# Optimization experiments

Hardware: AMD Instinct MI355X
Metric: run time of the kernel (lower is better)

The kernel has to match this reference:

```python
import jax, jax.numpy as jnp
import numpy as np

N_NODES = 100000
N_EDGES = 1600000
F_IN = 64
HIDDEN = 64
N_CLASSES = 2


def setup_inputs() -> dict:
    key = jax.random.key(0)
    k1, k2, k3, k4, k5, k6 = jax.random.split(key, 6)
    x = jax.random.normal(k1, (N_NODES, F_IN), dtype=jnp.float32)
    edge_index = jax.random.randint(k2, (2, N_EDGES), 0, N_NODES, dtype=jnp.int64)
    # Glorot-ish init for GCNConv linear weights, zero bias (PyG default)
    W1 = jax.random.normal(k3, (F_IN, HIDDEN), dtype=jnp.float32) * (1.0 / np.sqrt(F_IN))
    b1 = jnp.zeros((HIDDEN,), dtype=jnp.float32)
    W2 = jax.random.normal(k4, (HIDDEN, N_CLASSES), dtype=jnp.float32) * (1.0 / np.sqrt(HIDDEN))
    b2 = jnp.zeros((N_CLASSES,), dtype=jnp.float32)
    return {"x": x, "edge_index": edge_index, "W1": W1, "b1": b1, "W2": W2, "b2": b2}


def _gcn_norm(edge_index, num_nodes):
    # Add self-loops, then symmetric normalization D^-1/2 (A+I) D^-1/2
    loops = jnp.arange(num_nodes, dtype=edge_index.dtype)
    row = jnp.concatenate([edge_index[0], loops])  # [E+N] targets
    col = jnp.concatenate([edge_index[1], loops])  # [E+N] sources
    deg = jax.ops.segment_sum(jnp.ones(row.shape[0], jnp.float32), row, num_segments=num_nodes)
    dinv = jnp.where(deg > 0, jax.lax.rsqrt(deg), 0.0)
    norm = dinv[row] * dinv[col]  # [E+N]
    return row, col, norm


def _gcn_conv(x, W, b, row, col, norm, num_nodes):
    h = x @ W                                   # [N, out]
    msg = h[col] * norm[:, None]                # gather + scale, [E+N, out]
    agg = jax.ops.segment_sum(msg, row, num_segments=num_nodes)  # scatter-add
    return agg + b


def reference(x, edge_index, W1, b1, W2, b2):
    n = x.shape[0]
    row, col, norm = _gcn_norm(edge_index, n)
    h = jax.nn.relu(_gcn_conv(x, W1, b1, row, col, norm, n))
    # dropout p=0.5 is identity in eval mode
    logits = _gcn_conv(h, W2, b2, row, col, norm, n)
    return jax.nn.softmax(logits, axis=1)
```

## Files before the change

### kernel.cpp

```cpp
#include <hip/hip_runtime.h>
#include <hip/hip_fp16.h>


typedef _Float16 f16x8 __attribute__((ext_vector_type(8)));
typedef float f32x4 __attribute__((ext_vector_type(4)));

#define CAPSH 12
#define CAP (1 << CAPSH)
#define NBK 784

__global__ __launch_bounds__(256, 4) void k_binfused(const int* __restrict__ row,
                                                     const int* __restrict__ col,
                                                     int* __restrict__ relcur,
                                                     unsigned* __restrict__ pairbuf,
                                                     __half* __restrict__ hp,
                                                     const float* __restrict__ x,
                                                     const float* __restrict__ W1,
                                                     float* __restrict__ hf32,
                                                     int E, int nb, int N, int nTileB) {
    __shared__ unsigned items[4096];
    __shared__ unsigned short bktid[4096];
    __shared__ int cnt[NBK];
    __shared__ int start0[NBK];
    __shared__ int cursor[NBK];
    __shared__ int gbase[NBK];

    int tid = threadIdx.x;

    if (blockIdx.x < nTileB) {
        int base = blockIdx.x * 4096;
        int m = E - base; if (m > 4096) m = 4096;

        for (int t = tid; t < nb; t += 256) cnt[t] = 0;
        __syncthreads();
        for (int i = tid; i < m; i += 256) atomicAdd(&cnt[row[base + i] >> 7], 1);
        __syncthreads();
        if (tid < 64) {
            int lane = tid, running = 0;
            for (int ch = 0; ch < 13; ++ch) {
                int idx = ch * 64 + lane;
                int v = (idx < nb) ? cnt[idx] : 0;
                int s = v;
#pragma unroll
                for (int off = 1; off < 64; off <<= 1) {
                    int t = __shfl_up(s, off, 64);
                    if (lane >= off) s += t;
                }
                if (idx < nb) { start0[idx] = running + s - v; cursor[idx] = running + s - v; }
                running += __shfl(s, 63, 64);
            }
        }
        __syncthreads();
        for (int i = tid; i < m; i += 256) {
            int r = row[base + i];
            int c = col[base + i];
            int b = r >> 7;
            int pos = atomicAdd(&cursor[b], 1);
            items[pos] = ((unsigned)(r & 127) << 24) | (unsigned)c;
            bktid[pos] = (unsigned short)b;
        }
        __syncthreads();
        for (int t = tid; t < nb; t += 256) {
            int cv = cnt[t];
            if (cv > 0) gbase[t] = (t << CAPSH) + atomicAdd(&relcur[t], cv);
        }
        __syncthreads();
        for (int i = tid; i < m; i += 256) {
            int b = bktid[i];
            pairbuf[gbase[b] + (i - start0[b])] = items[i];
        }
        if (blockIdx.x == 0 && tid < 32) ((int*)(hp + (size_t)N * 64))[tid] = 0;
    } else {
        int g = blockIdx.x - nTileB;
        int n0 = g << 8;
        int lane = tid & 63, q = lane >> 4, mm = lane & 15;
        f16x8 bf[4][2];
#pragma unroll
        for (int nt = 0; nt < 4; ++nt)
#pragma unroll
            for (int kk = 0; kk < 2; ++kk)
#pragma unroll
                for (int j = 0; j < 8; ++j)
                    bf[nt][kk][j] = (_Float16)W1[(kk * 32 + q * 8 + j) * 64 + nt * 16 + mm];

        int nn = N - n0; if (nn > 256) nn = 256;
        for (int t = (tid >> 6); t < (nn >> 4); t += 4) {
            const float* xrow = x + (size_t)(n0 + t * 16 + mm) * 64;
            float4 u0 = *(const float4*)(xrow + q * 8);
            float4 u1 = *(const float4*)(xrow + q * 8 + 4);
            float4 u2 = *(const float4*)(xrow + 32 + q * 8);
            float4 u3 = *(const float4*)(xrow + 32 + q * 8 + 4);
            f16x8 a0, a1;
            a0[0] = (_Float16)u0.x; a0[1] = (_Float16)u0.y; a0[2] = (_Float16)u0.z; a0[3] = (_Float16)u0.w;
            a0[4] = (_Float16)u1.x; a0[5] = (_Float16)u1.y; a0[6] = (_Float16)u1.z; a0[7] = (_Float16)u1.w;
            a1[0] = (_Float16)u2.x; a1[1] = (_Float16)u2.y; a1[2] = (_Float16)u2.z; a1[3] = (_Float16)u2.w;
            a1[4] = (_Float16)u3.x; a1[5] = (_Float16)u3.y; a1[6] = (_Float16)u3.z; a1[7] = (_Float16)u3.w;
            f32x4 ac0 = {0.f, 0.f, 0.f, 0.f}, ac1 = ac0, ac2 = ac0, ac3 = ac0;
            ac0 = __builtin_amdgcn_mfma_f32_16x16x32_f16(a0, bf[0][0], ac0, 0, 0, 0);
            ac1 = __builtin_amdgcn_mfma_f32_16x16x32_f16(a0, bf[1][0], ac1, 0, 0, 0);
            ac2 = __builtin_amdgcn_mfma_f32_16x16x32_f16(a0, bf[2][0], ac2, 0, 0, 0);
            ac3 = __builtin_amdgcn_mfma_f32_16x16x32_f16(a0, bf[3][0], ac3, 0, 0, 0);
            ac0 = __builtin_amdgcn_mfma_f32_16x16x32_f16(a1, bf[0][1], ac0, 0, 0, 0);
            ac1 = __builtin_amdgcn_mfma_f32_16x16x32_f16(a1, bf[1][1], ac1, 0, 0, 0);
            ac2 = __builtin_amdgcn_mfma_f32_16x16x32_f16(a1, bf[2][1], ac2, 0, 0, 0);
            ac3 = __builtin_amdgcn_mfma_f32_16x16x32_f16(a1, bf[3][1], ac3, 0, 0, 0);
#pragma unroll
            for (int reg = 0; reg < 4; ++reg) {
                int rl = t * 16 + q * 4 + reg;
                float* dst = hf32 + (size_t)(n0 + rl) * 64 + mm;
                dst[0]  = ac0[reg];
                dst[16] = ac1[reg];
                dst[32] = ac2[reg];
                dst[48] = ac3[reg];
            }
        }
    }
}

__global__ __launch_bounds__(256, 4) void k_sortscale(const unsigned* __restrict__ pairbuf,
                                                      const int* __restrict__ relcur,
                                                      const float* __restrict__ hf32,
                                                      int* __restrict__ scol,
                                                      int* __restrict__ offsets,
                                                      int* __restrict__ deg,
                                                      float* __restrict__ dinv,
                                                      __half* __restrict__ hp,
                                                      int N, int nb) {
    __shared__ int cnt[256];
    __shared__ int spre[128];
    __shared__ int cur[128];
    __shared__ float sdinv[128];
    int b = blockIdx.x;
    int tid = threadIdx.x;
    int lo = b << CAPSH;
    int hi = lo + relcur[b];
    cnt[tid] = 0;
    __syncthreads();
    for (int i = lo + tid; i < hi; i += 256)
        atomicAdd(&cnt[pairbuf[i] >> 24], 1);
    __syncthreads();
    if (tid < 64) {
        int lane = tid, running = 0;
#pragma unroll
        for (int ch = 0; ch < 2; ++ch) {
            int idx = ch * 64 + lane;
            int v = cnt[idx];
            int s = v;
#pragma unroll
            for (int off = 1; off < 64; off <<= 1) {
                int t = __shfl_up(s, off, 64);
                if (lane >= off) s += t;
            }
            spre[idx] = running + s - v;
            running += __shfl(s, 63, 64);
        }
    }
    __syncthreads();
    int n0 = b << 7;
    if (tid < 128) {
        int cv = cnt[tid];
        int excl = spre[tid];
        int n = n0 + tid;
        float dv = rsqrtf((float)(cv + 1));
        if (n < N) { offsets[n] = lo + excl; deg[n] = cv; dinv[n] = dv; }
        sdinv[tid] = dv;
        cur[tid] = lo + excl;
    }
    if (b == 0 && tid == 0) {
        offsets[N] = 0; deg[N] = 0;
        scol[nb << CAPSH] = N;
    }
    __syncthreads();
    for (int i = lo + tid; i < hi; i += 256) {
        unsigned it = pairbuf[i];
        int pos = atomicAdd(&cur[it >> 24], 1);
        scol[pos] = (int)(it & 0xFFFFFFu);
    }
    int rowi = tid >> 1, half = tid & 1;
    int n = n0 + rowi;
    if (n < N) {
        float dv = sdinv[rowi];
        const float4* src = (const float4*)(hf32 + (size_t)n * 64 + half * 32);
        f16x8* dst = (f16x8*)(hp + (size_t)n * 64 + half * 32);
#pragma unroll
        for (int k = 0; k < 4; ++k) {
            float4 u0 = src[2 * k];
            float4 u1 = src[2 * k + 1];
            f16x8 o;
            o[0] = (_Float16)(dv * u0.x); o[1] = (_Float16)(dv * u0.y);
            o[2] = (_Float16)(dv * u0.z); o[3] = (_Float16)(dv * u0.w);
            o[4] = (_Float16)(dv * u1.x); o[5] = (_Float16)(dv * u1.y);
            o[6] = (_Float16)(dv * u1.z); o[7] = (_Float16)(dv * u1.w);
            dst[k] = o;
        }
    }
}

__global__ __launch_bounds__(256, 4) void k_agg1(const __half* __restrict__ hp,
                                                 const int* __restrict__ offsets,
                                                 const int* __restrict__ deg,
                                                 const int* __restrict__ scol,
                                                 const float* __restrict__ dinv,
                                                 const float* __restrict__ b1,
                                                 const float* __restrict__ W2,
                                                 float2* __restrict__ h2p,
                                                 int N, int SENT) {
    int lane = threadIdx.x & 63;
    int slot = lane >> 3;
    int chunk = lane & 7;
    int wid = (int)((blockIdx.x * 256 + threadIdx.x) >> 6);
    int n = wid * 8 + slot;
    int nc = (n < N) ? n : N;
    int start = offsets[nc];
    int dg = deg[nc];
    int maxd = dg;
#pragma unroll
    for (int s = 8; s <= 32; s <<= 1) {
        int o = __shfl_xor(maxd, s, 64);
        maxd = (o > maxd) ? o : maxd;
    }
    const float4* hp4 = (const float4*)hp;
    float4 sr = hp4[(size_t)nc * 8 + chunk];
    __half2 acc0 = ((const __half2*)&sr)[0];
    __half2 acc1 = ((const __half2*)&sr)[1];
    __half2 acc2 = ((const __half2*)&sr)[2];
    __half2 acc3 = ((const __half2*)&sr)[3];
    for (int j0 = 0; j0 < maxd; j0 += 8) {
        int c[8];
#pragma unroll
        for (int u = 0; u < 8; ++u)
            c[u] = scol[(j0 + u < dg) ? (start + j0 + u) : SENT];
        float4 r[8];
#pragma unroll
        for (int u = 0; u < 8; ++u) r[u] = hp4[(size_t)c[u] * 8 + chunk];
#pragma unroll
        for (int u = 0; u < 8; ++u) {
            const __half2* hh = (const __half2*)&r[u];
            acc0 = __hadd2(acc0, hh[0]); acc1 = __hadd2(acc1, hh[1]);
            acc2 = __hadd2(acc2, hh[2]); acc3 = __hadd2(acc3, hh[3]);
        }
    }
    float af[8];
    { float2 f;
      f = __half22float2(acc0); af[0] = f.x; af[1] = f.y;
      f = __half22float2(acc1); af[2] = f.x; af[3] = f.y;
      f = __half22float2(acc2); af[4] = f.x; af[5] = f.y;
      f = __half22float2(acc3); af[6] = f.x; af[7] = f.y; }
    float dn = dinv[(n < N) ? n : (N - 1)];
    float4 b1a = ((const float4*)b1)[chunk * 2];
    float4 b1b = ((const float4*)b1)[chunk * 2 + 1];
    float h1[8];
    h1[0] = fmaxf(fmaf(dn, af[0], b1a.x), 0.f);
    h1[1] = fmaxf(fmaf(dn, af[1], b1a.y), 0.f);
    h1[2] = fmaxf(fmaf(dn, af[2], b1a.z), 0.f);
    h1[3] = fmaxf(fmaf(dn, af[3], b1a.w), 0.f);
    h1[4] = fmaxf(fmaf(dn, af[4], b1b.x), 0.f);
    h1[5] = fmaxf(fmaf(dn, af[5], b1b.y), 0.f);
    h1[6] = fmaxf(fmaf(dn, af[6], b1b.z), 0.f);
    h1[7] = fmaxf(fmaf(dn, af[7], b1b.w), 0.f);
    float p0 = 0.f, p1 = 0.f;
#pragma unroll
    for (int k = 0; k < 4; ++k) {
        float4 w = ((const float4*)W2)[chunk * 4 + k];
        p0 = fmaf(h1[2 * k], w.x, p0); p1 = fmaf(h1[2 * k], w.y, p1);
        p0 = fmaf(h1[2 * k + 1], w.z, p0); p1 = fmaf(h1[2 * k + 1], w.w, p1);
    }
#pragma unroll
    for (int s = 1; s <= 4; s <<= 1) {
        p0 += __shfl_xor(p0, s, 64);
        p1 += __shfl_xor(p1, s, 64);
    }
    if (chunk == 0 && n < N) h2p[n] = make_float2(dn * p0, dn * p1);
}

__global__ __launch_bounds__(256) void k_agg2(const float2* __restrict__ h2p,
                                              const int* __restrict__ offsets,
                                              const int* __restrict__ deg,
                                              const int* __restrict__ scol,
                                              const float* __restrict__ dinv,
                                              const float* __restrict__ b2,
                                              float2* __restrict__ out, int N) {
    int gtid = blockIdx.x * 256 + threadIdx.x;
    int n = gtid >> 4;
    int sub = threadIdx.x & 15;
    if (n >= N) return;
    int start = offsets[n], end = start + deg[n];
    float ax = 0.f, ay = 0.f;
    if (sub == 0) { float2 s = h2p[n]; ax = s.x; ay = s.y; }
    for (int j = start + sub; j < end; j += 16) {
        float2 v = h2p[scol[j]];
        ax += v.x; ay += v.y;
    }
#pragma unroll
    for (int s = 1; s <= 8; s <<= 1) {
        ax += __shfl_xor(ax, s, 64);
        ay += __shfl_xor(ay, s, 64);
    }
    if (sub == 0) {
        float dn = dinv[n];
        float l0 = fmaf(dn, ax, b2[0]), l1 = fmaf(dn, ay, b2[1]);
        float m = fmaxf(l0, l1);
        float e0 = __expf(l0 - m), e1 = __expf(l1 - m);
        float inv = 1.0f / (e0 + e1);
        out[n] = make_float2(e0 * inv, e1 * inv);
    }
}

extern "C" void kernel_launch(void* const* d_in, const int* in_sizes, int n_in,
                              void* d_out, int out_size, void* d_ws, size_t ws_size,
                              hipStream_t stream) {
    const float* x  = (const float*)d_in[0];
    const int*   ei = (const int*)d_in[1];
    const float* W1 = (const float*)d_in[2];
    const float* b1 = (const float*)d_in[3];
    const float* W2 = (const float*)d_in[4];
    const float* b2 = (const float*)d_in[5];
    float2* out = (float2*)d_out;

    const int N = in_sizes[0] / 64;
    const int E = in_sizes[1] / 2;
    const int nb = (N + 127) >> 7;
    const int SENT = nb << CAPSH;
    const int* row = ei;
    const int* col = ei + E;

    char* p = (char*)d_ws;
    auto alloc = [&](size_t bytes) -> void* {
        void* r = (void*)p;
        p += (bytes + 255) & ~(size_t)255;
        return r;
    };
    int*   relcur  = (int*)alloc((size_t)nb * 4);
    int*   offsets = (int*)alloc((size_t)(N + 1) * 4);
    int*   deg     = (int*)alloc((size_t)(N + 1) * 4);
    float* dinv    = (float*)alloc((size_t)N * 4);
    unsigned* pairbuf = (unsigned*)alloc((size_t)nb * CAP * 4);
    int*   scol    = (int*)alloc(((size_t)nb * CAP + 1) * 4);
    __half* hp     = (__half*)alloc((size_t)(N + 1) * 64 * 2);
    float2* h2p    = (float2*)alloc((size_t)N * 8);
    float* hf32    = (float*)alloc((size_t)N * 64 * 4);

    const int nTileB = (E + 4095) / 4096;
    const int nGemm  = (N + 255) >> 8;

    hipMemsetAsync(relcur, 0, (size_t)nb * 4, stream);
    k_binfused<<<nTileB + nGemm, 256, 0, stream>>>(row, col, relcur, pairbuf, hp,
                                                   x, W1, hf32, E, nb, N, nTileB);
    k_sortscale<<<nb, 256, 0, stream>>>(pairbuf, relcur, hf32, scol, offsets, deg, dinv, hp, N, nb);
    const int nwaves = (N + 7) / 8;
    k_agg1<<<(nwaves + 3) / 4, 256, 0, stream>>>(hp, offsets, deg, scol, dinv, b1, W2, h2p, N, SENT);
    k_agg2<<<(N * 16 + 255) / 256, 256, 0, stream>>>(h2p, offsets, deg, scol, dinv, b2, out, N);
}
```

Measured before the change: 169.7 us.

## Write unscaled fp16 GEMM output directly and apply source dinv during aggregation

The GEMM stage now writes fp16 features straight into hp instead of an fp32 staging buffer. This removes the separate pass in the sort kernel that read hf32, scaled each row by dinv and wrote hp. In exchange, the first aggregation loads dinv for every neighbour index, gathering an extra 4 bytes per edge, and accumulates in fp32 with fma instead of half2 adds. This changes precision and adds per-edge scalar loads, and the GEMM output is now written as scattered 2-byte stores.

```diff
diff --git a/kernel.cpp b/kernel.cpp
--- a/kernel.cpp
+++ b/kernel.cpp
@@ -16,7 +16,6 @@
                                                      __half* __restrict__ hp,
                                                      const float* __restrict__ x,
                                                      const float* __restrict__ W1,
-                                                     float* __restrict__ hf32,
                                                      int E, int nb, int N, int nTileB) {
     __shared__ unsigned items[4096];
     __shared__ unsigned short bktid[4096];
@@ -107,29 +106,26 @@
 #pragma unroll
             for (int reg = 0; reg < 4; ++reg) {
                 int rl = t * 16 + q * 4 + reg;
-                float* dst = hf32 + (size_t)(n0 + rl) * 64 + mm;
-                dst[0]  = ac0[reg];
-                dst[16] = ac1[reg];
-                dst[32] = ac2[reg];
-                dst[48] = ac3[reg];
+                __half* dst = hp + (size_t)(n0 + rl) * 64 + mm;
+                dst[0]  = __float2half(ac0[reg]);
+                dst[16] = __float2half(ac1[reg]);
+                dst[32] = __float2half(ac2[reg]);
+                dst[48] = __float2half(ac3[reg]);
             }
         }
     }
 }
 
-__global__ __launch_bounds__(256, 4) void k_sortscale(const unsigned* __restrict__ pairbuf,
-                                                      const int* __restrict__ relcur,
-                                                      const float* __restrict__ hf32,
-                                                      int* __restrict__ scol,
-                                                      int* __restrict__ offsets,
-                                                      int* __restrict__ deg,
-                                                      float* __restrict__ dinv,
-                                                      __half* __restrict__ hp,
-                                                      int N, int nb) {
+__global__ __launch_bounds__(256, 4) void k_sort(const unsigned* __restrict__ pairbuf,
+                                                 const int* __restrict__ relcur,
+                                                 int* __restrict__ scol,
+                                                 int* __restrict__ offsets,
+                                                 int* __restrict__ deg,
+                                                 float* __restrict__ dinv,
+                                                 int N, int nb) {
     __shared__ int cnt[256];
     __shared__ int spre[128];
     __shared__ int cur[128];
-    __shared__ float sdinv[128];
     int b = blockIdx.x;
     int tid = threadIdx.x;
     int lo = b << CAPSH;
@@ -161,13 +157,16 @@
         int cv = cnt[tid];
         int excl = spre[tid];
         int n = n0 + tid;
-        float dv = rsqrtf((float)(cv + 1));
-        if (n < N) { offsets[n] = lo + excl; deg[n] = cv; dinv[n] = dv; }
-        sdinv[tid] = dv;
+        if (n < N) {
+            offsets[n] = lo + excl;
+            deg[n] = cv;
+            dinv[n] = rsqrtf((float)(cv + 1));
+        }
         cur[tid] = lo + excl;
     }
     if (b == 0 && tid == 0) {
         offsets[N] = 0; deg[N] = 0;
+        dinv[N] = 0.f;
         scol[nb << CAPSH] = N;
     }
     __syncthreads();
@@ -175,24 +174,6 @@
         unsigned it = pairbuf[i];
         int pos = atomicAdd(&cur[it >> 24], 1);
         scol[pos] = (int)(it & 0xFFFFFFu);
-    }
-    int rowi = tid >> 1, half = tid & 1;
-    int n = n0 + rowi;
-    if (n < N) {
-        float dv = sdinv[rowi];
-        const float4* src = (const float4*)(hf32 + (size_t)n * 64 + half * 32);
-        f16x8* dst = (f16x8*)(hp + (size_t)n * 64 + half * 32);
-#pragma unroll
-        for (int k = 0; k < 4; ++k) {
-            float4 u0 = src[2 * k];
-            float4 u1 = src[2 * k + 1];
-            f16x8 o;
-            o[0] = (_Float16)(dv * u0.x); o[1] = (_Float16)(dv * u0.y);
-            o[2] = (_Float16)(dv * u0.z); o[3] = (_Float16)(dv * u0.w);
-            o[4] = (_Float16)(dv * u1.x); o[5] = (_Float16)(dv * u1.y);
-            o[6] = (_Float16)(dv * u1.z); o[7] = (_Float16)(dv * u1.w);
-            dst[k] = o;
-        }
     }
 }
 
@@ -220,11 +201,18 @@
         maxd = (o > maxd) ? o : maxd;
     }
     const float4* hp4 = (const float4*)hp;
+    float dn = dinv[(n < N) ? n : (N - 1)];
     float4 sr = hp4[(size_t)nc * 8 + chunk];
-    __half2 acc0 = ((const __half2*)&sr)[0];
-    __half2 acc1 = ((const __half2*)&sr)[1];
-    __half2 acc2 = ((const __half2*)&sr)[2];
-    __half2 acc3 = ((const __half2*)&sr)[3];
+    float af[8];
+    {
+        const __half2* hh = (const __half2*)&sr;
+#pragma unroll
+        for (int k = 0; k < 4; ++k) {
+            float2 f = __half22float2(hh[k]);
+            af[2 * k]     = dn * f.x;
+            af[2 * k + 1] = dn * f.y;
+        }
+    }
     for (int j0 = 0; j0 < maxd; j0 += 8) {
         int c[8];
 #pragma unroll
@@ -233,20 +221,20 @@
         float4 r[8];
 #pragma unroll
         for (int u = 0; u < 8; ++u) r[u] = hp4[(size_t)c[u] * 8 + chunk];
+        float dv[8];
+#pragma unroll
+        for (int u = 0; u < 8; ++u) dv[u] = dinv[c[u]];
 #pragma unroll
         for (int u = 0; u < 8; ++u) {
             const __half2* hh = (const __half2*)&r[u];
-            acc0 = __hadd2(acc0, hh[0]); acc1 = __hadd2(acc1, hh[1]);
-            acc2 = __hadd2(acc2, hh[2]); acc3 = __hadd2(acc3, hh[3]);
-        }
-    }
-    float af[8];
-    { float2 f;
-      f = __half22float2(acc0); af[0] = f.x; af[1] = f.y;
-      f = __half22float2(acc1); af[2] = f.x; af[3] = f.y;
-      f = __half22float2(acc2); af[4] = f.x; af[5] = f.y;
-      f = __half22float2(acc3); af[6] = f.x; af[7] = f.y; }
-    float dn = dinv[(n < N) ? n : (N - 1)];
+#pragma unroll
+            for (int k = 0; k < 4; ++k) {
+                float2 f = __half22float2(hh[k]);
+                af[2 * k]     = fmaf(dv[u], f.x, af[2 * k]);
+                af[2 * k + 1] = fmaf(dv[u], f.y, af[2 * k + 1]);
+            }
+        }
+    }
     float4 b1a = ((const float4*)b1)[chunk * 2];
     float4 b1b = ((const float4*)b1)[chunk * 2 + 1];
     float h1[8];
@@ -333,20 +321,19 @@
     int*   relcur  = (int*)alloc((size_t)nb * 4);
     int*   offsets = (int*)alloc((size_t)(N + 1) * 4);
     int*   deg     = (int*)alloc((size_t)(N + 1) * 4);
-    float* dinv    = (float*)alloc((size_t)N * 4);
+    float* dinv    = (float*)alloc((size_t)(N + 1) * 4);
     unsigned* pairbuf = (unsigned*)alloc((size_t)nb * CAP * 4);
     int*   scol    = (int*)alloc(((size_t)nb * CAP + 1) * 4);
     __half* hp     = (__half*)alloc((size_t)(N + 1) * 64 * 2);
     float2* h2p    = (float2*)alloc((size_t)N * 8);
-    float* hf32    = (float*)alloc((size_t)N * 64 * 4);
 
     const int nTileB = (E + 4095) / 4096;
     const int nGemm  = (N + 255) >> 8;
 
     hipMemsetAsync(relcur, 0, (size_t)nb * 4, stream);
     k_binfused<<<nTileB + nGemm, 256, 0, stream>>>(row, col, relcur, pairbuf, hp,
-                                                   x, W1, hf32, E, nb, N, nTileB);
-    k_sortscale<<<nb, 256, 0, stream>>>(pairbuf, relcur, hf32, scol, offsets, deg, dinv, hp, N, nb);
+                                                   x, W1, E, nb, N, nTileB);
+    k_sort<<<nb, 256, 0, stream>>>(pairbuf, relcur, scol, offsets, deg, dinv, N, nb);
     const int nwaves = (N + 7) / 8;
     k_agg1<<<(nwaves + 3) / 4, 256, 0, stream>>>(hp, offsets, deg, scol, dinv, b1, W2, h2p, N, SENT);
     k_agg2<<<(N * 16 + 255) / 256, 256, 0, stream>>>(h2p, offsets, deg, scol, dinv, b2, out, N);
```

After: 165.8 us. 2.3% less time.
